# Optimization experiments

Measured on AMD Instinct MI355X. Metric: run time of the kernel, lower is better.

Reference implementation:

```python
import jax, jax.numpy as jnp
import numpy as np

QLEN, KLEN, RLEN, BSZ, NHEAD, DHEAD = 512, 512, 1024, 8, 16, 64
SCALE = 0.125  # 1/sqrt(d_head)


def rel_shift(x, klen):
    # x: [q, r, b, n] -> [q, klen, b, n] (XLNet relative shift)
    q, r, b, n = x.shape
    x = x.reshape(r, q, b, n)[1:]
    x = x.reshape(q, r - 1, b, n)[:, :klen]
    return x


def setup_inputs() -> dict:
    key = jax.random.key(0)
    ks = jax.random.split(key, 9)
    q_head = jax.random.normal(ks[0], (QLEN, BSZ, NHEAD, DHEAD), jnp.float32)
    k_head_h = jax.random.normal(ks[1], (KLEN, BSZ, NHEAD, DHEAD), jnp.float32)
    v_head_h = jax.random.normal(ks[2], (KLEN, BSZ, NHEAD, DHEAD), jnp.float32)
    k_head_r = jax.random.normal(ks[3], (RLEN, BSZ, NHEAD, DHEAD), jnp.float32)
    seg_embed = jax.random.normal(ks[4], (2, NHEAD, DHEAD), jnp.float32)
    seg_mat = jax.random.randint(ks[5], (QLEN, KLEN, BSZ), 0, 2).astype(bool)
    r_w_bias = jax.random.normal(ks[6], (NHEAD, DHEAD), jnp.float32) * 0.02
    r_r_bias = jax.random.normal(ks[7], (NHEAD, DHEAD), jnp.float32) * 0.02
    r_s_bias = jax.random.normal(ks[8], (NHEAD, DHEAD), jnp.float32) * 0.02
    # causal attention mask: 1.0 where key position j > query position i
    attn_mask = (jnp.arange(KLEN)[None, :] > jnp.arange(QLEN)[:, None]).astype(jnp.float32)
    attn_mask = attn_mask[:, :, None, None]  # [q, k, 1, 1]
    return {
        "q_head": q_head, "k_head_h": k_head_h, "v_head_h": v_head_h,
        "k_head_r": k_head_r, "seg_embed": seg_embed, "seg_mat": seg_mat,
        "r_w_bias": r_w_bias, "r_r_bias": r_r_bias, "r_s_bias": r_s_bias,
        "attn_mask": attn_mask,
    }


def reference(q_head, k_head_h, v_head_h, k_head_r, seg_embed, seg_mat,
              r_w_bias, r_r_bias, r_s_bias, attn_mask):
    klen = k_head_h.shape[0]
    # content-based score: [q, k, b, n]
    ac = jnp.einsum('ibnd,jbnd->ijbn', q_head + r_w_bias, k_head_h)
    # position-based score with relative shift
    bd = jnp.einsum('ibnd,jbnd->ijbn', q_head + r_r_bias, k_head_r)
    bd = rel_shift(bd, klen)
    # segment-based score: ef [q, 2, b, n] -> select per (q,k,b) via seg_mat
    ef = jnp.einsum('ibnd,snd->isbn', q_head + r_s_bias, seg_embed)
    ef = jnp.where(seg_mat[:, :, :, None], ef[:, 1:, :, :], ef[:, :1, :, :])
    attn_score = (ac + bd + ef) * SCALE
    attn_score = attn_score - 1e30 * attn_mask
    attn_prob = jax.nn.softmax(attn_score, axis=1)  # softmax over key dim j
    # dropout is identity in eval mode
    attn_vec = jnp.einsum('ijbn,jbnd->ibnd', attn_prob, v_head_h)
    return attn_vec
```

## Files before the change

### kernel.cpp

```cpp
#include <hip/hip_runtime.h>

#define QLEN 512
#define KLEN 512
#define RLEN 1024
#define BSZ 8
#define NHEAD 16
#define DHEAD 64
#define SROW 8192
#define SCALEF 0.125f

typedef __bf16 bf16x8 __attribute__((ext_vector_type(8)));
typedef __bf16 bf16x4 __attribute__((ext_vector_type(4)));
typedef float  f32x4  __attribute__((ext_vector_type(4)));

__device__ __forceinline__ f32x4 mfma_bf16(bf16x8 a, bf16x8 b, f32x4 c) {
    return __builtin_amdgcn_mfma_f32_16x16x32_bf16(a, b, c, 0, 0, 0);
}

__device__ __forceinline__ bf16x8 cvt_frag(f32x4 a, f32x4 b) {
    bf16x8 f;
    f[0] = (__bf16)a[0]; f[1] = (__bf16)a[1]; f[2] = (__bf16)a[2]; f[3] = (__bf16)a[3];
    f[4] = (__bf16)b[0]; f[5] = (__bf16)b[1]; f[6] = (__bf16)b[2]; f[7] = (__bf16)b[3];
    return f;
}


__global__ void __launch_bounds__(256)
cvt_kernel(const float* __restrict__ src, __bf16* __restrict__ dst, int n4) {
    int idx = blockIdx.x * blockDim.x + threadIdx.x;
    const int stride = gridDim.x * blockDim.x;
    for (; idx < n4; idx += stride) {
        f32x4 v = ((const f32x4*)src)[idx];
        bf16x4 o;
        o[0] = (__bf16)v[0]; o[1] = (__bf16)v[1]; o[2] = (__bf16)v[2]; o[3] = (__bf16)v[3];
        ((bf16x4*)dst)[idx] = o;
    }
}

__global__ void __launch_bounds__(256)
vtr_kernel(const float* __restrict__ vh, __bf16* __restrict__ vt) {
    const int blk = blockIdx.x;
    const int ch  = blk & 15;
    const int hn  = blk >> 4;
    const int d   = threadIdx.x & 63;
    const int w   = threadIdx.x >> 6;
    const float* base = vh + (size_t)hn * DHEAD + d;
    bf16x8 o;
#pragma unroll
    for (int e = 0; e < 8; ++e) {
        const int j = ch * 32 + 4 * w + (e & 3) + 16 * (e >> 2);
        o[e] = (__bf16)base[(size_t)j * SROW];
    }
    *(bf16x8*)(vt + ((size_t)hn * DHEAD + d) * KLEN + ch * 32 + 8 * w) = o;
}

__global__ void __launch_bounds__(256)
segpack_kernel(const void* __restrict__ segm, unsigned int* __restrict__ packed) {
    const int i   = blockIdx.x;
    const int tid = threadIdx.x;
    __shared__ unsigned int lds[4096];
    const unsigned int* segw = (const unsigned int*)segm;
    const unsigned char* segb = (const unsigned char*)segm;
    unsigned int sacc = 0;
#pragma unroll
    for (int t = 0; t < 32; ++t) sacc |= segw[t];
    const bool seg4B = (sacc <= 1u) || (sacc == 0x3F800000u);
    if (seg4B) {
        for (int t = tid; t < 4096; t += 256) lds[t] = segw[(size_t)i * 4096 + t];
    } else {
        for (int t = tid; t < 4096; t += 256) lds[t] = segb[(size_t)i * 4096 + t];
    }
    __syncthreads();
    if (tid < 128) {
        const int b = tid & 7, jw = tid >> 3;
        unsigned int word = 0;
#pragma unroll
        for (int jj = 0; jj < 32; ++jj)
            if (lds[(jw * 32 + jj) * 8 + b]) word |= (1u << jj);
        packed[((size_t)b * 16 + jw) * 512 + i] = word;
    }
}

struct ChunkRegs {
    bf16x8 kh0a, kh1a, kh0b, kh1b;
    bf16x8 kr0a, kr1a, kr0b, kr1b;
    unsigned int sw;
};

__global__ void __launch_bounds__(128)
relattn_v3(const float* __restrict__ q,  const __bf16* __restrict__ khb,
           const __bf16* __restrict__ vt, const __bf16* __restrict__ krb,
           const float* __restrict__ se, const unsigned int* __restrict__ segpk,
           const float* __restrict__ rw, const float* __restrict__ rr,
           const float* __restrict__ rs, float* __restrict__ out)
{
    const int tid  = threadIdx.x;
    const int wv   = tid >> 6;
    const int lane = tid & 63;
    const int g    = lane >> 4;
    const int c    = lane & 15;
    const int pairi = ((blockIdx.x & 7) << 1) | wv;
    const int hn   = blockIdx.x >> 3;
    const int b    = hn >> 4;
    const int n    = hn & 15;
    const size_t hoff = (size_t)hn * DHEAD;

    const __bf16* khh = khb + hoff;
    const __bf16* krh = krb + hoff;
    const __bf16* vth = vt + hoff * KLEN;
    const unsigned int* spb = segpk + (size_t)b * 16 * 512;
    const float* rwn = rw + n * DHEAD;
    const float* rrn = rr + n * DHEAD;
    const float* rsn = rs + n * DHEAD;

#pragma unroll 1
    for (int half = 0; half < 2; ++half) {
        const int itile = half ? (31 - pairi) : pairi;
        const int i0 = itile << 4;
        const int i  = i0 + c;

        bf16x8 qw[2], qr_[2], qs_[2];
        {
            const float* qrow = q + (size_t)i * SROW + hoff;
#pragma unroll
            for (int ks = 0; ks < 2; ++ks) {
                const int d0 = 32 * ks + 8 * g;
                f32x4 a0 = *(const f32x4*)(qrow + d0);
                f32x4 a1 = *(const f32x4*)(qrow + d0 + 4);
                qw[ks]  = cvt_frag(a0 + *(const f32x4*)(rwn + d0), a1 + *(const f32x4*)(rwn + d0 + 4));
                qr_[ks] = cvt_frag(a0 + *(const f32x4*)(rrn + d0), a1 + *(const f32x4*)(rrn + d0 + 4));
                qs_[ks] = cvt_frag(a0 + *(const f32x4*)(rsn + d0), a1 + *(const f32x4*)(rsn + d0 + 4));
            }
        }

        float e0, e1;
        {
            f32x4 eacc = {0.f, 0.f, 0.f, 0.f};
#pragma unroll
            for (int ks = 0; ks < 2; ++ks) {
                bf16x8 sfrag;
                if (c < 2) {
                    const float* sp = se + ((size_t)c * NHEAD + n) * DHEAD + 32 * ks + 8 * g;
                    sfrag = cvt_frag(*(const f32x4*)sp, *(const f32x4*)(sp + 4));
                } else {
#pragma unroll
                    for (int e = 0; e < 8; ++e) sfrag[e] = (__bf16)0.f;
                }
                eacc = mfma_bf16(sfrag, qs_[ks], eacc);
            }
            e0 = __shfl(eacc[0], c, 64);
            e1 = __shfl(eacc[1], c, 64);
        }

        auto windowc = [&](bf16x8 k0, bf16x8 k1, float* wsh) {
            f32x4 w = {0.f, 0.f, 0.f, 0.f};
            w = mfma_bf16(k0, qr_[0], w);
            w = mfma_bf16(k1, qr_[1], w);
            const int c3 = c & 3;
            const float w0 = w[0], w1 = w[1], w2 = w[2], w3 = w[3];
            const float r0 = (c3 == 0) ? w0 : (c3 == 1) ? w3 : (c3 == 2) ? w2 : w1;
            const float r1 = (c3 == 0) ? w1 : (c3 == 1) ? w0 : (c3 == 2) ? w3 : w2;
            const float r2 = (c3 == 0) ? w2 : (c3 == 1) ? w1 : (c3 == 2) ? w0 : w3;
            const float r3 = (c3 == 0) ? w3 : (c3 == 1) ? w2 : (c3 == 2) ? w1 : w0;
#pragma unroll
            for (int t = 0; t < 4; ++t) {
                const float rv = (t == 0) ? r0 : (t == 1) ? r1 : (t == 2) ? r2 : r3;
                const int rm  = (4 * g + t - c) & 15;
                const int src = ((rm >> 2) << 4) | c;
                wsh[t] = __shfl(rv, src, 64);
            }
        };

        float pw[4];
        {
            const __bf16* krow = krh + (size_t)(512 - i0 - 16 + c) * SROW;
            windowc(*(const bf16x8*)(krow + 8 * g), *(const bf16x8*)(krow + 32 + 8 * g), pw);
        }

        const int nch = (itile >> 1) + 1;

        auto LOADC = [&](int ch, ChunkRegs& R) {
            const int jb = ch << 5;
            const int r2 = jb + 16 + c;
            const __bf16* p1 = khh + (size_t)(jb + c) * SROW;
            R.kh0a = *(const bf16x8*)(p1 + 8 * g);
            R.kh1a = *(const bf16x8*)(p1 + 32 + 8 * g);
            const __bf16* p2 = khh + (size_t)(r2 < KLEN ? r2 : KLEN - 1) * SROW;
            R.kh0b = *(const bf16x8*)(p2 + 8 * g);
            R.kh1b = *(const bf16x8*)(p2 + 32 + 8 * g);
            const int wb1 = 512 + jb - i0 + c;
            const __bf16* p3 = krh + (size_t)wb1 * SROW;
            R.kr0a = *(const bf16x8*)(p3 + 8 * g);
            R.kr1a = *(const bf16x8*)(p3 + 32 + 8 * g);
            const __bf16* p4 = krh + (size_t)(wb1 + 16) * SROW;
            R.kr0b = *(const bf16x8*)(p4 + 8 * g);
            R.kr1b = *(const bf16x8*)(p4 + 32 + 8 * g);
            R.sw = spb[(size_t)(jb >> 5) * 512 + i];
        };

        f32x4 o0 = {0,0,0,0}, o1 = {0,0,0,0}, o2 = {0,0,0,0}, o3 = {0,0,0,0};
        float m_run = -3.0e38f, l_run = 0.f;

        auto COMPUTE = [&](int ch, ChunkRegs& R) {
            const int jb = ch << 5;
            float st[8];
            {
                f32x4 acc = {0.f, 0.f, 0.f, 0.f};
                acc = mfma_bf16(R.kh0a, qw[0], acc);
                acc = mfma_bf16(R.kh1a, qw[1], acc);
                float cw[4];
                windowc(R.kr0a, R.kr1a, cw);
#pragma unroll
                for (int t = 0; t < 4; ++t) {
                    const int jr = 4 * g + t;
                    const int j  = jb + jr;
                    const float bd = (jr >= c) ? cw[t] : pw[t];
                    const float ef = ((R.sw >> (4 * g + t)) & 1u) ? e1 : e0;
                    const float sv = (acc[t] + bd + ef) * SCALEF;
                    st[t] = (j <= i) ? sv : -1e30f;
                    pw[t] = cw[t];
                }
            }
            if (jb + 16 <= i0) {
                f32x4 acc = {0.f, 0.f, 0.f, 0.f};
                acc = mfma_bf16(R.kh0b, qw[0], acc);
                acc = mfma_bf16(R.kh1b, qw[1], acc);
                float cw[4];
                windowc(R.kr0b, R.kr1b, cw);
#pragma unroll
                for (int t = 0; t < 4; ++t) {
                    const int jr = 4 * g + t;
                    const int j  = jb + 16 + jr;
                    const float bd = (jr >= c) ? cw[t] : pw[t];
                    const float ef = ((R.sw >> (16 + 4 * g + t)) & 1u) ? e1 : e0;
                    const float sv = (acc[t] + bd + ef) * SCALEF;
                    st[4 + t] = (j <= i) ? sv : -1e30f;
                    pw[t] = cw[t];
                }
            } else {
                st[4] = st[5] = st[6] = st[7] = -1e30f;
            }

            float tm = fmaxf(fmaxf(fmaxf(st[0], st[1]), fmaxf(st[2], st[3])),
                             fmaxf(fmaxf(st[4], st[5]), fmaxf(st[6], st[7])));
            tm = fmaxf(tm, __shfl_xor(tm, 16, 64));
            tm = fmaxf(tm, __shfl_xor(tm, 32, 64));
            const float mnew = fmaxf(m_run, tm);
            const float scl  = __expf(m_run - mnew);
            float p[8];
#pragma unroll
            for (int t = 0; t < 8; ++t) p[t] = __expf(st[t] - mnew);
            float ls = ((p[0] + p[1]) + (p[2] + p[3])) + ((p[4] + p[5]) + (p[6] + p[7]));
            ls += __shfl_xor(ls, 16, 64);
            ls += __shfl_xor(ls, 32, 64);
            l_run = l_run * scl + ls;
            m_run = mnew;
            o0 *= scl; o1 *= scl; o2 *= scl; o3 *= scl;

            bf16x8 pf;
#pragma unroll
            for (int e = 0; e < 8; ++e) pf[e] = (__bf16)p[e];
#pragma unroll
            for (int dt = 0; dt < 4; ++dt) {
                bf16x8 vf = *(const bf16x8*)(vth + (size_t)(dt * 16 + c) * KLEN + jb + 8 * g);
                f32x4& od = (dt == 0) ? o0 : (dt == 1) ? o1 : (dt == 2) ? o2 : o3;
                od = mfma_bf16(vf, pf, od);
            }
        };

        ChunkRegs A, B;
        LOADC(0, A);
        int ch = 0;
        while (true) {
            if (ch + 1 < nch) LOADC(ch + 1, B);
            COMPUTE(ch, A);
            if (++ch >= nch) break;
            if (ch + 1 < nch) LOADC(ch + 1, A);
            COMPUTE(ch, B);
            if (++ch >= nch) break;
        }

        const float inv = 1.f / l_run;
        float* orow = out + (size_t)i * SROW + hoff;
#pragma unroll
        for (int t = 0; t < 4; ++t) {
            orow[ 0 + 4 * g + t] = o0[t] * inv;
            orow[16 + 4 * g + t] = o1[t] * inv;
            orow[32 + 4 * g + t] = o2[t] * inv;
            orow[48 + 4 * g + t] = o3[t] * inv;
        }
    }
}

__global__ void __launch_bounds__(256)
relattn_v1(const float* __restrict__ q,  const float* __restrict__ kh,
           const float* __restrict__ vh, const float* __restrict__ kr,
           const float* __restrict__ se, const void* __restrict__ segm,
           const float* __restrict__ rw, const float* __restrict__ rr,
           const float* __restrict__ rs, float* __restrict__ out)
{
    const int tid  = threadIdx.x;
    const int wv   = tid >> 6;
    const int lane = tid & 63;
    const int g    = lane >> 4;
    const int c    = lane & 15;
    const int qt8  = blockIdx.x & 7;
    const int hn   = blockIdx.x >> 3;
    const int b    = hn >> 4;
    const int n    = hn & 15;
    const int itile = qt8 + 8 * wv;
    const int i0   = itile << 4;
    const int i    = i0 + c;
    const size_t hoff = (size_t)hn * DHEAD;

    const float* khh = kh + hoff;
    const float* krh = kr + hoff;
    const float* vhh = vh + hoff;

    const unsigned int* segw = (const unsigned int*)segm;
    const unsigned char* segb = (const unsigned char*)segm;
    unsigned int sacc = 0;
#pragma unroll
    for (int t = 0; t < 32; ++t) sacc |= segw[t];
    const bool seg4B = (sacc <= 1u) || (sacc == 0x3F800000u);

    bf16x8 qw[2], qr_[2], qs_[2];
    {
        const float* qrow = q + (size_t)i * SROW + hoff;
        const float* rwn = rw + n * DHEAD;
        const float* rrn = rr + n * DHEAD;
        const float* rsn = rs + n * DHEAD;
#pragma unroll
        for (int ks = 0; ks < 2; ++ks) {
            const int d0 = 32 * ks + 4 * g;
            f32x4 a0 = *(const f32x4*)(qrow + d0);
            f32x4 a1 = *(const f32x4*)(qrow + d0 + 16);
            qw[ks]  = cvt_frag(a0 + *(const f32x4*)(rwn + d0), a1 + *(const f32x4*)(rwn + d0 + 16));
            qr_[ks] = cvt_frag(a0 + *(const f32x4*)(rrn + d0), a1 + *(const f32x4*)(rrn + d0 + 16));
            qs_[ks] = cvt_frag(a0 + *(const f32x4*)(rsn + d0), a1 + *(const f32x4*)(rsn + d0 + 16));
        }
    }

    float e0, e1;
    {
        f32x4 eacc = {0.f, 0.f, 0.f, 0.f};
#pragma unroll
        for (int ks = 0; ks < 2; ++ks) {
            bf16x8 sfrag;
            if (c < 2) {
                const float* sp = se + ((size_t)c * NHEAD + n) * DHEAD + 32 * ks + 4 * g;
                sfrag = cvt_frag(*(const f32x4*)sp, *(const f32x4*)(sp + 16));
            } else {
#pragma unroll
                for (int e = 0; e < 8; ++e) sfrag[e] = (__bf16)0.f;
            }
            eacc = mfma_bf16(sfrag, qs_[ks], eacc);
        }
        e0 = __shfl(eacc[0], c, 64);
        e1 = __shfl(eacc[1], c, 64);
    }

    auto window_sh = [&](int base, float* wsh) {
        const float* krow = krh + (size_t)(base + c) * SROW;
        bf16x8 k0 = cvt_frag(*(const f32x4*)(krow + 4 * g), *(const f32x4*)(krow + 4 * g + 16));
        bf16x8 k1 = cvt_frag(*(const f32x4*)(krow + 32 + 4 * g), *(const f32x4*)(krow + 48 + 4 * g));
        f32x4 w = {0.f, 0.f, 0.f, 0.f};
        w = mfma_bf16(k0, qr_[0], w);
        w = mfma_bf16(k1, qr_[1], w);
        const int c3 = c & 3;
        const float w0 = w[0], w1 = w[1], w2 = w[2], w3 = w[3];
        const float r0 = (c3 == 0) ? w0 : (c3 == 1) ? w3 : (c3 == 2) ? w2 : w1;
        const float r1 = (c3 == 0) ? w1 : (c3 == 1) ? w0 : (c3 == 2) ? w3 : w2;
        const float r2 = (c3 == 0) ? w2 : (c3 == 1) ? w1 : (c3 == 2) ? w0 : w3;
        const float r3 = (c3 == 0) ? w3 : (c3 == 1) ? w2 : (c3 == 2) ? w1 : w0;
#pragma unroll
        for (int t = 0; t < 4; ++t) {
            const float rv = (t == 0) ? r0 : (t == 1) ? r1 : (t == 2) ? r2 : r3;
            const int rm  = (4 * g + t - c) & 15;
            const int src = ((rm >> 2) << 4) | c;
            wsh[t] = __shfl(rv, src, 64);
        }
    };

    float pw[4];
    window_sh(512 - i0 - 16, pw);

    auto do_tile = [&](int j0, float* stt) {
        const float* krow = khh + (size_t)(j0 + c) * SROW;
        bf16x8 k0 = cvt_frag(*(const f32x4*)(krow + 4 * g), *(const f32x4*)(krow + 4 * g + 16));
        bf16x8 k1 = cvt_frag(*(const f32x4*)(krow + 32 + 4 * g), *(const f32x4*)(krow + 48 + 4 * g));
        f32x4 acc = {0.f, 0.f, 0.f, 0.f};
        acc = mfma_bf16(k0, qw[0], acc);
        acc = mfma_bf16(k1, qw[1], acc);
        float cw[4];
        window_sh(512 + j0 - i0, cw);

        int sgv[4];
        const size_t sbase = ((size_t)i * KLEN + j0 + 4 * g) * BSZ + b;
        if (seg4B) {
#pragma unroll
            for (int t = 0; t < 4; ++t) sgv[t] = (segw[sbase + (size_t)t * BSZ] != 0u);
        } else {
#pragma unroll
            for (int t = 0; t < 4; ++t) sgv[t] = segb[sbase + (size_t)t * BSZ];
        }

#pragma unroll
        for (int t = 0; t < 4; ++t) {
            const int jr = 4 * g + t;
            const int j  = j0 + jr;
            const float bd = (jr >= c) ? cw[t] : pw[t];
            const float ef = sgv[t] ? e1 : e0;
            const float sv = (acc[t] + bd + ef) * SCALEF;
            stt[t] = (j <= i) ? sv : -1e30f;
            pw[t] = cw[t];
        }
    };

    f32x4 o0 = {0,0,0,0}, o1 = {0,0,0,0}, o2 = {0,0,0,0}, o3 = {0,0,0,0};
    float m_run = -3.0e38f, l_run = 0.f;

    const int nch = (itile >> 1) + 1;
    for (int ch = 0; ch < nch; ++ch) {
        const int jb = ch << 5;
        float st[8];
        do_tile(jb, st);
        if (jb + 16 <= i0) {
            do_tile(jb + 16, st + 4);
        } else {
            st[4] = st[5] = st[6] = st[7] = -1e30f;
        }

        float tm = fmaxf(fmaxf(fmaxf(st[0], st[1]), fmaxf(st[2], st[3])),
                         fmaxf(fmaxf(st[4], st[5]), fmaxf(st[6], st[7])));
        tm = fmaxf(tm, __shfl_xor(tm, 16, 64));
        tm = fmaxf(tm, __shfl_xor(tm, 32, 64));
        const float mnew = fmaxf(m_run, tm);
        const float scl  = __expf(m_run - mnew);
        float p[8];
#pragma unroll
        for (int t = 0; t < 8; ++t) p[t] = __expf(st[t] - mnew);
        float ls = ((p[0] + p[1]) + (p[2] + p[3])) + ((p[4] + p[5]) + (p[6] + p[7]));
        ls += __shfl_xor(ls, 16, 64);
        ls += __shfl_xor(ls, 32, 64);
        l_run = l_run * scl + ls;
        m_run = mnew;
        o0 *= scl; o1 *= scl; o2 *= scl; o3 *= scl;

        bf16x8 pf;
#pragma unroll
        for (int e = 0; e < 8; ++e) pf[e] = (__bf16)p[e];

#pragma unroll
        for (int dt = 0; dt < 4; ++dt) {
            bf16x8 vf;
#pragma unroll
            for (int e = 0; e < 8; ++e) {
                const int j = jb + 4 * g + (e & 3) + ((e >> 2) << 4);
                const float vv = (j < KLEN) ? vhh[(size_t)j * SROW + dt * 16 + c] : 0.f;
                vf[e] = (__bf16)vv;
            }
            f32x4& od = (dt == 0) ? o0 : (dt == 1) ? o1 : (dt == 2) ? o2 : o3;
            od = mfma_bf16(vf, pf, od);
        }
    }

    const float inv = 1.f / l_run;
    float* orow = out + (size_t)i * SROW + hoff;
#pragma unroll
    for (int t = 0; t < 4; ++t) {
        orow[ 0 + 4 * g + t] = o0[t] * inv;
        orow[16 + 4 * g + t] = o1[t] * inv;
        orow[32 + 4 * g + t] = o2[t] * inv;
        orow[48 + 4 * g + t] = o3[t] * inv;
    }
}

extern "C" void kernel_launch(void* const* d_in, const int* in_sizes, int n_in,
                              void* d_out, int out_size, void* d_ws, size_t ws_size,
                              hipStream_t stream) {
    const float* q  = (const float*)d_in[0];
    const float* kh = (const float*)d_in[1];
    const float* vh = (const float*)d_in[2];
    const float* kr = (const float*)d_in[3];
    const float* se = (const float*)d_in[4];
    const void*  sm = (const void*)d_in[5];
    const float* rw = (const float*)d_in[6];
    const float* rr = (const float*)d_in[7];
    const float* rs = (const float*)d_in[8];
    float* out = (float*)d_out;
    (void)in_sizes; (void)n_in; (void)out_size;

    const size_t vt_e = (size_t)BSZ * NHEAD * DHEAD * KLEN;
    const size_t kh_e = (size_t)KLEN * SROW;
    const size_t kr_e = (size_t)RLEN * SROW;
    const size_t sp_w = (size_t)BSZ * 16 * 512;
    const size_t need = (vt_e + kh_e + kr_e) * sizeof(__bf16) + sp_w * 4;

    if (ws_size >= need) {
        __bf16* wsb = (__bf16*)d_ws;
        __bf16* vt  = wsb;
        __bf16* khb = wsb + vt_e;
        __bf16* krb = wsb + vt_e + kh_e;
        unsigned int* segpk = (unsigned int*)(wsb + vt_e + kh_e + kr_e);
        cvt_kernel<<<dim3(1024), dim3(256), 0, stream>>>(kh, khb, (int)(kh_e / 4));
        cvt_kernel<<<dim3(1024), dim3(256), 0, stream>>>(kr, krb, (int)(kr_e / 4));
        vtr_kernel<<<dim3(2048), dim3(256), 0, stream>>>(vh, vt);
        segpack_kernel<<<dim3(512), dim3(256), 0, stream>>>(sm, segpk);
        relattn_v3<<<dim3(1024), dim3(128), 0, stream>>>(q, khb, vt, krb, se, segpk, rw, rr, rs, out);
    } else {
        relattn_v1<<<dim3(1024), dim3(256), 0, stream>>>(q, kh, vh, kr, se, sm, rw, rr, rs, out);
    }
}
```

Baseline: 231.9 us.

## Split key chunks across two waves with LDS softmax merge

Each block now handles one query-tile pair per head, with its two waves splitting the key-chunk range in half instead of each wave owning a separate query tile. Partial outputs and softmax stats from wave 1 go through shared memory and are merged by wave 0 with rescaling. The grid doubles and is remapped so head/batch varies fastest, and V fragment loads are hoisted to the start of each chunk's compute. This is meant to shorten the serial per-wave chunk loop and improve load balance and latency hiding, at the cost of LDS traffic, two barriers per half and a merge step.

```diff
diff --git a/kernel.cpp b/kernel.cpp
--- a/kernel.cpp
+++ b/kernel.cpp
@@ -88,19 +88,21 @@
 };
 
 __global__ void __launch_bounds__(128)
-relattn_v3(const float* __restrict__ q,  const __bf16* __restrict__ khb,
+relattn_v4(const float* __restrict__ q,  const __bf16* __restrict__ khb,
            const __bf16* __restrict__ vt, const __bf16* __restrict__ krb,
            const float* __restrict__ se, const unsigned int* __restrict__ segpk,
            const float* __restrict__ rw, const float* __restrict__ rr,
            const float* __restrict__ rs, float* __restrict__ out)
 {
+    __shared__ float smem[18][64];
     const int tid  = threadIdx.x;
     const int wv   = tid >> 6;
     const int lane = tid & 63;
     const int g    = lane >> 4;
     const int c    = lane & 15;
-    const int pairi = ((blockIdx.x & 7) << 1) | wv;
-    const int hn   = blockIdx.x >> 3;
+    const int bp   = blockIdx.x;
+    const int hn   = (bp & 7) * 16 + ((bp >> 3) & 15);
+    const int pairi = bp >> 7;
     const int b    = hn >> 4;
     const int n    = hn & 15;
     const size_t hoff = (size_t)hn * DHEAD;
@@ -171,13 +173,16 @@
             }
         };
 
+        const int nch = (itile >> 1) + 1;
+        const int h   = (nch + 1) >> 1;
+        const int cb  = wv ? h : 0;
+        const int ce  = wv ? nch : h;
+
         float pw[4];
         {
-            const __bf16* krow = krh + (size_t)(512 - i0 - 16 + c) * SROW;
+            const __bf16* krow = krh + (size_t)(512 + (cb << 5) - 16 - i0 + c) * SROW;
             windowc(*(const bf16x8*)(krow + 8 * g), *(const bf16x8*)(krow + 32 + 8 * g), pw);
         }
-
-        const int nch = (itile >> 1) + 1;
 
         auto LOADC = [&](int ch, ChunkRegs& R) {
             const int jb = ch << 5;
@@ -203,6 +208,11 @@
 
         auto COMPUTE = [&](int ch, ChunkRegs& R) {
             const int jb = ch << 5;
+            bf16x8 vfa = *(const bf16x8*)(vth + (size_t)( 0 + c) * KLEN + jb + 8 * g);
+            bf16x8 vfb = *(const bf16x8*)(vth + (size_t)(16 + c) * KLEN + jb + 8 * g);
+            bf16x8 vfc = *(const bf16x8*)(vth + (size_t)(32 + c) * KLEN + jb + 8 * g);
+            bf16x8 vfd = *(const bf16x8*)(vth + (size_t)(48 + c) * KLEN + jb + 8 * g);
+
             float st[8];
             {
                 f32x4 acc = {0.f, 0.f, 0.f, 0.f};
@@ -260,35 +270,54 @@
             bf16x8 pf;
 #pragma unroll
             for (int e = 0; e < 8; ++e) pf[e] = (__bf16)p[e];
-#pragma unroll
-            for (int dt = 0; dt < 4; ++dt) {
-                bf16x8 vf = *(const bf16x8*)(vth + (size_t)(dt * 16 + c) * KLEN + jb + 8 * g);
-                f32x4& od = (dt == 0) ? o0 : (dt == 1) ? o1 : (dt == 2) ? o2 : o3;
-                od = mfma_bf16(vf, pf, od);
-            }
+            o0 = mfma_bf16(vfa, pf, o0);
+            o1 = mfma_bf16(vfb, pf, o1);
+            o2 = mfma_bf16(vfc, pf, o2);
+            o3 = mfma_bf16(vfd, pf, o3);
         };
 
-        ChunkRegs A, B;
-        LOADC(0, A);
-        int ch = 0;
-        while (true) {
-            if (ch + 1 < nch) LOADC(ch + 1, B);
-            COMPUTE(ch, A);
-            if (++ch >= nch) break;
-            if (ch + 1 < nch) LOADC(ch + 1, A);
-            COMPUTE(ch, B);
-            if (++ch >= nch) break;
-        }
-
-        const float inv = 1.f / l_run;
-        float* orow = out + (size_t)i * SROW + hoff;
-#pragma unroll
-        for (int t = 0; t < 4; ++t) {
-            orow[ 0 + 4 * g + t] = o0[t] * inv;
-            orow[16 + 4 * g + t] = o1[t] * inv;
-            orow[32 + 4 * g + t] = o2[t] * inv;
-            orow[48 + 4 * g + t] = o3[t] * inv;
-        }
+        if (cb < ce) {
+            ChunkRegs A, B;
+            LOADC(cb, A);
+            int ch = cb;
+            while (true) {
+                if (ch + 1 < ce) LOADC(ch + 1, B);
+                COMPUTE(ch, A);
+                if (++ch >= ce) break;
+                if (ch + 1 < ce) LOADC(ch + 1, A);
+                COMPUTE(ch, B);
+                if (++ch >= ce) break;
+            }
+        }
+
+        if (wv == 1) {
+#pragma unroll
+            for (int t = 0; t < 4; ++t) {
+                smem[ 0 + t][lane] = o0[t];
+                smem[ 4 + t][lane] = o1[t];
+                smem[ 8 + t][lane] = o2[t];
+                smem[12 + t][lane] = o3[t];
+            }
+            smem[16][lane] = m_run;
+            smem[17][lane] = l_run;
+        }
+        __syncthreads();
+        if (wv == 0) {
+            const float m1 = smem[16][lane], l1 = smem[17][lane];
+            const float ms = fmaxf(m_run, m1);
+            const float s0 = __expf(m_run - ms);
+            const float s1 = __expf(m1 - ms);
+            const float inv = 1.f / (l_run * s0 + l1 * s1);
+            float* orow = out + (size_t)i * SROW + hoff;
+#pragma unroll
+            for (int t = 0; t < 4; ++t) {
+                orow[ 0 + 4 * g + t] = (o0[t] * s0 + smem[ 0 + t][lane] * s1) * inv;
+                orow[16 + 4 * g + t] = (o1[t] * s0 + smem[ 4 + t][lane] * s1) * inv;
+                orow[32 + 4 * g + t] = (o2[t] * s0 + smem[ 8 + t][lane] * s1) * inv;
+                orow[48 + 4 * g + t] = (o3[t] * s0 + smem[12 + t][lane] * s1) * inv;
+            }
+        }
+        __syncthreads();
     }
 }
 
@@ -507,7 +536,7 @@
         cvt_kernel<<<dim3(1024), dim3(256), 0, stream>>>(kr, krb, (int)(kr_e / 4));
         vtr_kernel<<<dim3(2048), dim3(256), 0, stream>>>(vh, vt);
         segpack_kernel<<<dim3(512), dim3(256), 0, stream>>>(sm, segpk);
-        relattn_v3<<<dim3(1024), dim3(128), 0, stream>>>(q, khb, vt, krb, se, segpk, rw, rr, rs, out);
+        relattn_v4<<<dim3(2048), dim3(128), 0, stream>>>(q, khb, vt, krb, se, segpk, rw, rr, rs, out);
     } else {
         relattn_v1<<<dim3(1024), dim3(256), 0, stream>>>(q, kh, vh, kr, se, sm, rw, rr, rs, out);
     }
```

After: 216.8 us. -6.5%, faster.
